# Performance work log

Hardware: AMD Instinct MI355X
Metric: run time of the kernel (lower is better)

Reference implementation:

```python
import jax, jax.numpy as jnp
import numpy as np

B, N, D, H, PSI = 8, 7225, 256, 8, 64
DH = D // H
DF = 4 * D
EPS = 1e-5


def _ln(x, g, b):
    m = jnp.mean(x, axis=-1, keepdims=True)
    v = jnp.mean((x - m) ** 2, axis=-1, keepdims=True)
    return (x - m) / jnp.sqrt(v + EPS) * g + b


def _gelu(x):
    return jax.nn.gelu(x, approximate=False)


def setup_inputs() -> dict:
    key = jax.random.key(0)
    ks = jax.random.split(key, 16)
    w = lambda k, s: (jax.random.normal(k, s, dtype=jnp.float32) * 0.02)
    inp = {
        'x': jax.random.normal(ks[0], (B, N, D), dtype=jnp.float32),
        'fx': jax.random.normal(ks[1], (B, N, D), dtype=jnp.float32),
        'ln1_g': jnp.ones((D,), jnp.float32), 'ln1_b': jnp.zeros((D,), jnp.float32),
        'Wq': w(ks[2], (D, D)), 'Wk': w(ks[3], (D, D)), 'Wv': w(ks[4], (D, D)),
        'Wo': w(ks[5], (D, D)), 'bo': jnp.zeros((D,), jnp.float32),
        'ln2_g': jnp.ones((D,), jnp.float32), 'ln2_b': jnp.zeros((D,), jnp.float32),
        'mlp_W1': w(ks[6], (D, DF)), 'mlp_b1': jnp.zeros((DF,), jnp.float32),
        'mlp_W2': w(ks[7], (DF, D)), 'mlp_b2': jnp.zeros((D,), jnp.float32),
        'proj_W1': w(ks[8], (D, D)), 'proj_b1': jnp.zeros((D,), jnp.float32),
        'proj_W2': w(ks[9], (D, PSI)), 'proj_b2': jnp.zeros((PSI,), jnp.float32),
        'mu': jnp.zeros((PSI,), jnp.float32),
        'ln3_g': jnp.ones((D,), jnp.float32), 'ln3_b': jnp.zeros((D,), jnp.float32),
        'mlp2_W1': w(ks[10], (D, DF)), 'mlp2_b1': jnp.zeros((DF,), jnp.float32),
        'mlp2_W2': w(ks[11], (DF, D)), 'mlp2_b2': jnp.zeros((D,), jnp.float32),
    }
    return inp


def _forward(x, fx, ln1_g, ln1_b, Wq, Wk, Wv, Wo, bo, ln2_g, ln2_b,
             mlp_W1, mlp_b1, mlp_W2, mlp_b2, proj_W1, proj_b1, proj_W2, proj_b2,
             mu, ln3_g, ln3_b, mlp2_W1, mlp2_b1, mlp2_W2, mlp2_b2):
    # --- linear (kernelized, non-causal) self-attention ---
    h = _ln(x, ln1_g, ln1_b)
    to_heads = lambda t: t.reshape(B, N, H, DH).transpose(0, 2, 1, 3)  # bhnd
    q = to_heads(h @ Wq)
    k = to_heads(h @ Wk)
    v = to_heads(h @ Wv)
    q = jax.nn.softmax(q, axis=-1) * (DH ** -0.5)   # feature-dim softmax
    k = jax.nn.softmax(k, axis=-2)                  # sequence-dim softmax
    ctx = jnp.einsum('bhnd,bhne->bhde', k, v)       # [B,H,DH,DH]
    attn = jnp.einsum('bhnd,bhde->bhne', q, ctx)    # [B,H,N,DH]
    attn = attn.transpose(0, 2, 1, 3).reshape(B, N, D) @ Wo + bo
    x = attn + x

    # --- MLP block (n_layers=0, no residual inside MLP) ---
    h = _ln(x, ln2_g, ln2_b)
    x = _gelu(h @ mlp_W1 + mlp_b1) @ mlp_W2 + mlp_b2 + x

    # --- low-rank projection + covariance whitening (orth=True, training path) ---
    x_ = _gelu(x @ proj_W1 + proj_b1) @ proj_W2 + proj_b2       # [B,N,PSI]
    cov = jnp.einsum('blc,bld->cd', x_, x_) / (B * N)           # [PSI,PSI]
    L = jnp.linalg.cholesky(cov)
    L_inv_T = jnp.linalg.inv(L).T
    x_ = x_ @ L_inv_T

    # --- softplus-scaled low-rank operator on fx ---
    ctx2 = jnp.einsum('blp,bld->bpd', x_, fx)                   # [B,PSI,D]
    fx = jnp.einsum('blp,bpd->bld', x_ * jax.nn.softplus(mu), ctx2)

    fx = _gelu(_ln(fx, ln3_g, ln3_b) @ mlp2_W1 + mlp2_b1) @ mlp2_W2 + mlp2_b2
    return x, fx


def reference(x, fx, ln1_g, ln1_b, Wq, Wk, Wv, Wo, bo, ln2_g, ln2_b,
              mlp_W1, mlp_b1, mlp_W2, mlp_b2, proj_W1, proj_b1, proj_W2, proj_b2,
              mu, ln3_g, ln3_b, mlp2_W1, mlp2_b1, mlp2_W2, mlp2_b2):
    return _forward(x, fx, ln1_g, ln1_b, Wq, Wk, Wv, Wo, bo, ln2_g, ln2_b,
                    mlp_W1, mlp_b1, mlp_W2, mlp_b2, proj_W1, proj_b1, proj_W2, proj_b2,
                    mu, ln3_g, ln3_b, mlp2_W1, mlp2_b1, mlp2_W2, mlp2_b2)
```

## Files before the change

kernel.cpp:

```cpp
#include <hip/hip_runtime.h>
#include <math.h>

typedef unsigned short u16;
typedef unsigned int u32;
typedef float f32x4 __attribute__((ext_vector_type(4)));
typedef __bf16 bf16x8 __attribute__((ext_vector_type(8)));

#define NTOK 57800
#define NSEQ 7225
#define NBATCH 8

static __device__ __forceinline__ float bf2f(u16 u){ u32 x=((u32)u)<<16; float f; __builtin_memcpy(&f,&x,4); return f; }
static __device__ __forceinline__ u16 f2bf(float f){ __bf16 h = (__bf16)f; u16 u; __builtin_memcpy(&u,&h,2); return u; }
static __device__ __forceinline__ float gelu_f(float v){
  float t = v * v;
  float w = fmaf(t, -0.07135481627f, -1.5957691216f);
  float e = __expf(w * v);
  return v * __builtin_amdgcn_rcpf(1.0f + e);
}

static __device__ __forceinline__ void gl16(const u16* g, u16* l){
  __builtin_amdgcn_global_load_lds((const __attribute__((address_space(1))) void*)g,
                                   (__attribute__((address_space(3))) void*)l, 16, 0, 0);
}

static __device__ __forceinline__ float rdlane(float v, int lane){
  int i; __builtin_memcpy(&i,&v,4);
  int r = __builtin_amdgcn_readlane(i, lane);
  float f; __builtin_memcpy(&f,&r,4);
  return f;
}

struct WJobs { const float* src[10]; u16* dst[10]; int K[10]; int N[10]; };
__global__ __launch_bounds__(256) void wtrans_all(WJobs j){
  int z = blockIdx.z;
  int K = j.K[z], N = j.N[z];
  int bk = blockIdx.x*32, bn = blockIdx.y*32;
  if (bk >= K || bn >= N) return;
  const float* src = j.src[z];
  u16* dst = j.dst[z];
  __shared__ float t[32][33];
  int tx = threadIdx.x&31, ty = threadIdx.x>>5;
  #pragma unroll
  for (int u=0;u<4;u++){
    int k = bk+ty+u*8, n = bn+tx;
    if (k<K && n<N) t[ty+u*8][tx] = src[(long)k*N+n];
  }
  __syncthreads();
  #pragma unroll
  for (int u=0;u<4;u++){
    int n = bn+ty+u*8, k = bk+tx;
    if (n<N && k<K) dst[(long)n*K+k] = f2bf(t[tx][ty+u*8]);
  }
}

__global__ __launch_bounds__(256) void ln_kernel(const float* __restrict__ in, const float* __restrict__ g,
                                                 const float* __restrict__ b, u16* __restrict__ out, int rows){
  int wid = threadIdx.x>>6, lane = threadIdx.x&63;
  int row = blockIdx.x*4 + wid;
  if (row >= rows) return;
  const float4 xv = *reinterpret_cast<const float4*>(in + (long)row*256 + lane*4);
  float s = xv.x+xv.y+xv.z+xv.w;
  float s2 = xv.x*xv.x+xv.y*xv.y+xv.z*xv.z+xv.w*xv.w;
  #pragma unroll
  for (int o=32;o;o>>=1){ s += __shfl_xor(s,o,64); s2 += __shfl_xor(s2,o,64); }
  float mean = s*(1.f/256.f);
  float var = fmaxf(s2*(1.f/256.f) - mean*mean, 0.f);
  float rstd = rsqrtf(var + 1e-5f);
  float4 gv = *reinterpret_cast<const float4*>(g + lane*4);
  float4 bv = *reinterpret_cast<const float4*>(b + lane*4);
  ushort4 o4;
  o4.x = f2bf((xv.x-mean)*rstd*gv.x + bv.x);
  o4.y = f2bf((xv.y-mean)*rstd*gv.y + bv.y);
  o4.z = f2bf((xv.z-mean)*rstd*gv.z + bv.z);
  o4.w = f2bf((xv.w-mean)*rstd*gv.w + bv.w);
  *reinterpret_cast<ushort4*>(out + (long)row*256 + lane*4) = o4;
}

template<bool BIASF, bool RESF, bool GELUF, bool OF32, bool OBF16>
__global__ __launch_bounds__(256) void gemm3(const u16* __restrict__ A, const u16* __restrict__ Bt,
    const float* __restrict__ bias, const float* __restrict__ resid,
    float* __restrict__ outF, u16* __restrict__ outB,
    int M, int N, int K, int gn, long aB, long bB, long cB)
{
  __shared__ __align__(16) u16 lds[2][8192];
  int nwg = gridDim.x, bid = blockIdx.x;
  int qx = nwg>>3, rx = nwg&7;
  int xcd = bid&7, lin = bid>>3;
  int swz = (xcd<rx)? (xcd*(qx+1)+lin) : (rx + xcd*qx + lin);
  int mi_ = swz/gn;
  int m0 = mi_*128, n0 = (swz - mi_*gn)*128;

  const u16* Ab  = A  + (long)blockIdx.z*aB;
  const u16* Btb = Bt + (long)blockIdx.z*bB;
  long coff = (long)blockIdx.z*cB;
  int tid = threadIdx.x, w = tid>>6, l = tid&63;
  int lr = l>>3;
  int csrc = (((l&7) ^ lr) << 3);
  int l15 = l&15, lq = l>>4;
  int wm = (w>>1)*64, wn = (w&1)*64;
  int sx = (l15&7)<<3;

  f32x4 acc[4][4];
  #pragma unroll
  for (int a=0;a<4;a++)
    #pragma unroll
    for (int b2=0;b2<4;b2++)
      #pragma unroll
      for (int r2=0;r2<4;r2++) acc[a][b2][r2]=0.f;

  int nt = K>>6;

  auto STAGE = [&](int k0){
    #pragma unroll
    for (int u=0;u<4;u++){
      int rr = w*32 + u*8;
      gl16(Ab  + (long)(m0+rr+lr)*K + k0 + csrc, &lds[0][0] + rr*64 + l*8);
      gl16(Btb + (long)(n0+rr+lr)*K + k0 + csrc, &lds[1][0] + rr*64 + l*8);
    }
  };

  STAGE(0);
  for (int t=0;;t++){
    __syncthreads();
    #pragma unroll
    for (int ks=0;ks<2;ks++){
      bf16x8 af[4], bfv[4];
      int ko = ks*32 + lq*8;
      #pragma unroll
      for (int mi=0;mi<4;mi++)
        af[mi]  = *reinterpret_cast<const bf16x8*>(&lds[0][0] + (wm+mi*16+l15)*64 + (ko ^ sx));
      #pragma unroll
      for (int ni=0;ni<4;ni++)
        bfv[ni] = *reinterpret_cast<const bf16x8*>(&lds[1][0] + (wn+ni*16+l15)*64 + (ko ^ sx));
      #pragma unroll
      for (int mi=0;mi<4;mi++)
        #pragma unroll
        for (int ni=0;ni<4;ni++)
          acc[mi][ni] = __builtin_amdgcn_mfma_f32_16x16x32_bf16(bfv[ni], af[mi], acc[mi][ni], 0,0,0);
    }
    if (t+1 == nt) break;
    __syncthreads();
    STAGE((t+1)<<6);
  }

  #pragma unroll
  for (int mi=0;mi<4;mi++){
    int row = m0 + wm + mi*16 + l15;
    if (row >= M) continue;
    #pragma unroll
    for (int ni=0;ni<4;ni++){
      int col0 = n0 + wn + ni*16 + lq*4;
      if (col0 >= N) continue;
      f32x4 v = acc[mi][ni];
      if (BIASF){
        const float4 bv = *reinterpret_cast<const float4*>(bias + col0);
        v[0]+=bv.x; v[1]+=bv.y; v[2]+=bv.z; v[3]+=bv.w;
      }
      long idx = (long)row*N + col0;
      if (RESF){
        const float4 rv = *reinterpret_cast<const float4*>(resid + coff + idx);
        v[0]+=rv.x; v[1]+=rv.y; v[2]+=rv.z; v[3]+=rv.w;
      }
      if (GELUF){
        #pragma unroll
        for (int r2=0;r2<4;r2++) v[r2] = gelu_f(v[r2]);
      }
      if (OF32){
        float4 o; o.x=v[0]; o.y=v[1]; o.z=v[2]; o.w=v[3];
        *reinterpret_cast<float4*>(outF + coff + idx) = o;
      }
      if (OBF16){
        ushort4 o; o.x=f2bf(v[0]); o.y=f2bf(v[1]); o.z=f2bf(v[2]); o.w=f2bf(v[3]);
        *reinterpret_cast<ushort4*>(outB + coff + idx) = o;
      }
    }
  }
}

template<bool RESF, bool OBF16>
__global__ __launch_bounds__(256) void mlp_fused(const u16* __restrict__ A,
    const u16* __restrict__ W1t, const float* __restrict__ b1,
    const u16* __restrict__ W2t, const float* __restrict__ b2,
    const float* __restrict__ resid, float* __restrict__ outF, u16* __restrict__ outB, int M)
{
  __shared__ __align__(16) u16 hA[4][4096];
  __shared__ __align__(16) u16 P[2][4096];
  int nwg = gridDim.x, bid = blockIdx.x;
  int qx = nwg>>3, rx = nwg&7;
  int xcd = bid&7, lin = bid>>3;
  int swz = (xcd<rx)? (xcd*(qx+1)+lin) : (rx + xcd*qx + lin);
  int m0 = swz*64;

  int tid = threadIdx.x, w = tid>>6, l = tid&63;
  int lr = l>>3;
  int csrc = (((l&7) ^ lr) << 3);
  int l15 = l&15, lq = l>>4;
  int sx = (l15&7)<<3;
  int jn1 = w*32;
  int nn2 = w*64;

  #pragma unroll
  for (int kc=0; kc<4; kc++){
    #pragma unroll
    for (int u=0; u<2; u++){
      int rr = w*16 + u*8;
      gl16(A + (long)(m0+rr+lr)*256 + kc*64 + csrc, &hA[kc][0] + rr*64 + l*8);
    }
  }

  f32x4 acc2[4][4];
  #pragma unroll
  for (int a=0;a<4;a++)
    #pragma unroll
    for (int b_=0;b_<4;b_++)
      #pragma unroll
      for (int r=0;r<4;r++) acc2[a][b_][r]=0.f;

  asm volatile("s_waitcnt vmcnt(0)" ::: "memory");
  __syncthreads();

  #pragma unroll 1
  for (int jb=0; jb<8; jb++){
    f32x4 acc1[4][2];
    #pragma unroll
    for (int a=0;a<4;a++)
      #pragma unroll
      for (int b_=0;b_<2;b_++)
        #pragma unroll
        for (int r=0;r<4;r++) acc1[a][b_][r]=0.f;
    __builtin_amdgcn_s_setprio(1);
    #pragma unroll
    for (int kc=0;kc<4;kc++){
      #pragma unroll
      for (int ks=0;ks<2;ks++){
        int ko = ks*32 + lq*8;
        bf16x8 af[4], bfv[2];
        #pragma unroll
        for (int ni=0;ni<2;ni++){
          int jrow = jb*128 + jn1 + ni*16 + l15;
          bfv[ni] = *reinterpret_cast<const bf16x8*>(W1t + (long)jrow*256 + kc*64 + ko);
        }
        #pragma unroll
        for (int mi=0;mi<4;mi++)
          af[mi] = *reinterpret_cast<const bf16x8*>(&hA[kc][0] + (mi*16+l15)*64 + (ko ^ sx));
        #pragma unroll
        for (int mi=0;mi<4;mi++)
          #pragma unroll
          for (int ni=0;ni<2;ni++)
            acc1[mi][ni] = __builtin_amdgcn_mfma_f32_16x16x32_bf16(bfv[ni], af[mi], acc1[mi][ni], 0,0,0);
      }
    }
    __builtin_amdgcn_s_setprio(0);
    #pragma unroll
    for (int mi=0;mi<4;mi++){
      int row = mi*16 + l15;
      #pragma unroll
      for (int ni=0;ni<2;ni++){
        int jj = jn1 + ni*16 + lq*4;
        const float4 bv = *reinterpret_cast<const float4*>(b1 + jb*128 + jj);
        f32x4 v = acc1[mi][ni];
        v[0] = gelu_f(v[0]+bv.x); v[1] = gelu_f(v[1]+bv.y);
        v[2] = gelu_f(v[2]+bv.z); v[3] = gelu_f(v[3]+bv.w);
        ushort4 o; o.x=f2bf(v[0]); o.y=f2bf(v[1]); o.z=f2bf(v[2]); o.w=f2bf(v[3]);
        int c = jj & 63, ch = jj >> 6;
        *reinterpret_cast<ushort4*>(&P[ch][0] + row*64 + (c ^ ((row&7)<<3))) = o;
      }
    }
    __syncthreads();
    __builtin_amdgcn_s_setprio(1);
    #pragma unroll
    for (int kk=0;kk<4;kk++){
      int ko = (kk&1)*32 + lq*8;
      int ch = kk>>1;
      bf16x8 af2[4], bf2v[4];
      #pragma unroll
      for (int ni=0;ni<4;ni++){
        int nrow = nn2 + ni*16 + l15;
        bf2v[ni] = *reinterpret_cast<const bf16x8*>(W2t + (long)nrow*1024 + jb*128 + kk*32 + lq*8);
      }
      #pragma unroll
      for (int mi=0;mi<4;mi++)
        af2[mi] = *reinterpret_cast<const bf16x8*>(&P[ch][0] + (mi*16+l15)*64 + (ko ^ sx));
      #pragma unroll
      for (int mi=0;mi<4;mi++)
        #pragma unroll
        for (int ni=0;ni<4;ni++)
          acc2[mi][ni] = __builtin_amdgcn_mfma_f32_16x16x32_bf16(bf2v[ni], af2[mi], acc2[mi][ni], 0,0,0);
    }
    __builtin_amdgcn_s_setprio(0);
    __syncthreads();
  }

  #pragma unroll
  for (int mi=0;mi<4;mi++){
    int row = m0 + mi*16 + l15;
    if (row >= M) continue;
    #pragma unroll
    for (int ni=0;ni<4;ni++){
      int col = nn2 + ni*16 + lq*4;
      f32x4 v = acc2[mi][ni];
      const float4 bv = *reinterpret_cast<const float4*>(b2 + col);
      v[0]+=bv.x; v[1]+=bv.y; v[2]+=bv.z; v[3]+=bv.w;
      long idx = (long)row*256 + col;
      if (RESF){
        const float4 rv = *reinterpret_cast<const float4*>(resid + idx);
        v[0]+=rv.x; v[1]+=rv.y; v[2]+=rv.z; v[3]+=rv.w;
      }
      float4 o; o.x=v[0]; o.y=v[1]; o.z=v[2]; o.w=v[3];
      *reinterpret_cast<float4*>(outF + idx) = o;
      if (OBF16){
        ushort4 ob; ob.x=f2bf(v[0]); ob.y=f2bf(v[1]); ob.z=f2bf(v[2]); ob.w=f2bf(v[3]);
        *reinterpret_cast<ushort4*>(outB + idx) = ob;
      }
    }
  }
}

__global__ __launch_bounds__(256) void ctx_part(const u16* __restrict__ qkvb, float* __restrict__ part,
                                                float* __restrict__ spart2){
  int ch = blockIdx.x, bh = blockIdx.y; int b = bh>>3, h = bh&7;
  __shared__ float ek[8][32], vl[8][32];
  int tid = threadIdx.x;
  int d = tid&31, eg = (tid>>5)*4;
  float acc[4] = {0.f,0.f,0.f,0.f};
  float ssum = 0.f;
  int n0 = ch*226; int n1 = n0+226; if (n1 > NSEQ) n1 = NSEQ;
  for (int nb=n0; nb<n1; nb+=8){
    #pragma unroll
    for (int u=0;u<2;u++){
      int idx = tid + u*256; int r = idx>>6, c = idx&63;
      int n = nb + r;
      if (c < 32) ek[r][c]    = (n<n1)? __expf(bf2f(qkvb[((long)(b*NSEQ+n))*768 + 256 + h*32 + c])) : 0.f;
      else        vl[r][c-32] = (n<n1)? bf2f(qkvb[((long)(b*NSEQ+n))*768 + 512 + h*32 + (c-32)]) : 0.f;
    }
    __syncthreads();
    #pragma unroll
    for (int r=0;r<8;r++){
      float kv = ek[r][d];
      ssum += kv;
      #pragma unroll
      for (int j=0;j<4;j++) acc[j] += kv * vl[r][eg+j];
    }
    __syncthreads();
  }
  #pragma unroll
  for (int j=0;j<4;j++) part[((long)(bh*32+ch))*1024 + d*32 + eg + j] = acc[j];
  if (tid < 32) spart2[(bh*32+ch)*32 + d] = ssum;
}
__global__ void ctx_red(const float* __restrict__ part, const float* __restrict__ spart2,
                        float* __restrict__ ctx){
  int bh = blockIdx.x;
  __shared__ float sinvl[32];
  int tid = threadIdx.x;
  if (tid < 32){
    float s=0.f;
    for (int ch=0;ch<32;ch++) s += spart2[(bh*32+ch)*32 + tid];
    sinvl[tid] = 1.0f/s;
  }
  __syncthreads();
  for (int idx=tid; idx<1024; idx+=256){
    float s=0.f;
    for (int ch=0;ch<32;ch++) s += part[((long)(bh*32+ch))*1024 + idx];
    ctx[(long)bh*1024 + idx] = s * sinvl[idx>>5];
  }
}

__global__ __launch_bounds__(256) void qsoftmax(const u16* __restrict__ qkvb, u16* __restrict__ qsb){
  int wid = threadIdx.x>>6, lane = threadIdx.x&63;
  int n = blockIdx.x*4 + wid;
  int b = blockIdx.y;
  if (n >= NSEQ) return;
  const ushort4 qv = *reinterpret_cast<const ushort4*>(qkvb + ((long)(b*NSEQ+n))*768 + lane*4);
  float e0 = __expf(bf2f(qv.x)), e1 = __expf(bf2f(qv.y)),
        e2 = __expf(bf2f(qv.z)), e3 = __expf(bf2f(qv.w));
  float s = e0+e1+e2+e3;
  s += __shfl_xor(s,1,64); s += __shfl_xor(s,2,64); s += __shfl_xor(s,4,64);
  float r = 0.17677669529663687f / s;
  ushort4 o; o.x=f2bf(e0*r); o.y=f2bf(e1*r); o.z=f2bf(e2*r); o.w=f2bf(e3*r);
  *reinterpret_cast<ushort4*>(qsb + ((long)(b*NSEQ+n))*256 + lane*4) = o;
}

__global__ __launch_bounds__(256) void ctx_wo(const float* __restrict__ ctx, const u16* __restrict__ wot,
                                              u16* __restrict__ w2bt){
  int jg = blockIdx.x, b = blockIdx.y;
  int j0 = jg*32;
  __shared__ u16 wol[32][256];
  int tid = threadIdx.x;
  {
    int r = tid>>3, c = (tid&7)*32;
    const uint4* src = reinterpret_cast<const uint4*>(wot + (j0+r)*256 + c);
    uint4* dst = reinterpret_cast<uint4*>(&wol[r][c]);
    dst[0]=src[0]; dst[1]=src[1]; dst[2]=src[2]; dst[3]=src[3];
  }
  int h = tid>>5, d = tid&31;
  float creg[32];
  {
    const float4* cp = reinterpret_cast<const float4*>(ctx + (long)(b*8+h)*1024 + d*32);
    #pragma unroll
    for (int u=0;u<8;u++){ float4 v = cp[u]; creg[u*4]=v.x; creg[u*4+1]=v.y; creg[u*4+2]=v.z; creg[u*4+3]=v.w; }
  }
  __syncthreads();
  for (int jj=0;jj<32;jj++){
    const uint4* wp = reinterpret_cast<const uint4*>(&wol[jj][h*32]);
    float acc = 0.f;
    #pragma unroll
    for (int u=0;u<4;u++){
      uint4 wv = wp[u];
      acc += bf2f((u16)(wv.x&0xffffu))*creg[u*8+0] + bf2f((u16)(wv.x>>16))*creg[u*8+1]
           + bf2f((u16)(wv.y&0xffffu))*creg[u*8+2] + bf2f((u16)(wv.y>>16))*creg[u*8+3]
           + bf2f((u16)(wv.z&0xffffu))*creg[u*8+4] + bf2f((u16)(wv.z>>16))*creg[u*8+5]
           + bf2f((u16)(wv.w&0xffffu))*creg[u*8+6] + bf2f((u16)(wv.w>>16))*creg[u*8+7];
    }
    w2bt[((long)b*256 + j0+jj)*256 + tid] = f2bf(acc);
  }
}

__global__ __launch_bounds__(256) void cov_part(const float* __restrict__ xu, float* __restrict__ part){
  int ch = blockIdx.x;
  __shared__ float xl[2][8][64];
  int tid = threadIdx.x;
  int i = tid&63, jg = (tid>>6)*16;
  int lrow = tid>>5, lcol = (tid&31)*2;
  float acc[16];
  #pragma unroll
  for (int j=0;j<16;j++) acc[j]=0.f;
  int n0 = ch*113;
  const int NT = 15;
  float2 xr2;
  auto LOAD = [&](int t){
    int n = n0 + t*8 + lrow;
    if (n < n0+113 && n < NTOK) xr2 = *reinterpret_cast<const float2*>(xu + (long)n*64 + lcol);
    else { xr2.x = 0.f; xr2.y = 0.f; }
  };
  LOAD(0);
  for (int t=0; t<NT; t++){
    int cur = t&1;
    xl[cur][lrow][lcol] = xr2.x; xl[cur][lrow][lcol+1] = xr2.y;
    __syncthreads();
    if (t+1 < NT) LOAD(t+1);
    #pragma unroll
    for (int r=0;r<8;r++){
      float xv = xl[cur][r][i];
      const float4* fb = reinterpret_cast<const float4*>(&xl[cur][r][jg]);
      float4 f0=fb[0], f1=fb[1], f2=fb[2], f3=fb[3];
      acc[0]+=xv*f0.x; acc[1]+=xv*f0.y; acc[2]+=xv*f0.z; acc[3]+=xv*f0.w;
      acc[4]+=xv*f1.x; acc[5]+=xv*f1.y; acc[6]+=xv*f1.z; acc[7]+=xv*f1.w;
      acc[8]+=xv*f2.x; acc[9]+=xv*f2.y; acc[10]+=xv*f2.z; acc[11]+=xv*f2.w;
      acc[12]+=xv*f3.x; acc[13]+=xv*f3.y; acc[14]+=xv*f3.z; acc[15]+=xv*f3.w;
    }
    __syncthreads();
  }
  #pragma unroll
  for (int j=0;j<16;j++) part[(long)ch*4096 + (jg+j)*64 + i] = acc[j];
}
__global__ void cov_red(const float* __restrict__ part, float* __restrict__ cov){
  __shared__ float red[4][64];
  int o = blockIdx.x*64 + (threadIdx.x&63);
  int sl = threadIdx.x>>6;
  float s=0.f;
  for (int ch=sl; ch<512; ch+=4) s += part[(long)ch*4096 + o];
  if (sl>0) red[sl][threadIdx.x&63] = s;
  __syncthreads();
  if (sl==0){
    s += red[1][threadIdx.x&63] + red[2][threadIdx.x&63] + red[3][threadIdx.x&63];
    cov[o] = s * (1.0f/57800.0f);
  }
}

__global__ __launch_bounds__(64) void chol_inv(const float* __restrict__ cov, float* __restrict__ Linv){
  int t = threadIdx.x;
  float r[64];
  #pragma unroll
  for (int k=0;k<16;k++){
    float4 v4 = *reinterpret_cast<const float4*>(cov + (long)t*64 + k*4);
    r[k*4]=v4.x; r[k*4+1]=v4.y; r[k*4+2]=v4.z; r[k*4+3]=v4.w;
  }
  float dinv[64];
  #pragma unroll
  for (int j=0;j<64;j++){
    float ajj = rdlane(r[j], j);
    float ljj = sqrtf(fmaxf(ajj, 1e-20f));
    float rinv = 1.0f / ljj;
    dinv[j] = rinv;
    float ltj = r[j] * rinv;
    r[j] = ltj;
    #pragma unroll
    for (int k=j+1;k<64;k++){
      float lkj = rdlane(ltj, k);
      r[k] -= ltj * lkj;
    }
  }
  float v[64];
  #pragma unroll
  for (int k=0;k<64;k++) v[k] = (k==t) ? 1.f : 0.f;
  #pragma unroll
  for (int i=0;i<64;i++){
    float xi = v[i] * dinv[i];
    Linv[i*64 + t] = xi;
    #pragma unroll
    for (int k=i+1;k<64;k++){
      v[k] -= rdlane(r[i], k) * xi;
    }
  }
}

__global__ __launch_bounds__(256) void whiten(const float* __restrict__ xu, const float* __restrict__ Linv,
                                              const float* __restrict__ mu, u16* __restrict__ xw, u16* __restrict__ xws){
  __shared__ float Ll[64][65];
  int tid = threadIdx.x;
  for (int u=0; u<16; u++){ int idx = u*256+tid; Ll[idx>>6][idx&63] = Linv[idx]; }
  __syncthreads();
  int wid = tid>>6, lane = tid&63;
  float m = mu[lane];
  float sp = (m > 20.f)? m : log1pf(expf(m));
  for (int rr=0; rr<4; rr++){
    int row = blockIdx.x*16 + wid*4 + rr;
    if (row >= NTOK) continue;
    float xj = xu[(long)row*64 + lane];
    float s = 0.f;
    #pragma unroll
    for (int j=0;j<64;j++) s += __shfl(xj, j, 64) * Ll[lane][j];
    xw[(long)row*64+lane]  = f2bf(s);
    xws[(long)row*64+lane] = f2bf(s * sp);
  }
}

__global__ __launch_bounds__(512) void ctx2_part(const u16* __restrict__ xw, const float* __restrict__ fx,
                                                 float* __restrict__ part){
  int ch = blockIdx.x, b = blockIdx.y;
  __shared__ float xwlf[2][16][64];
  __shared__ float fxl[2][16][256];
  int tid = threadIdx.x;
  int p = tid&63, jg = ((tid>>6)&7)*32;
  int lrow = tid>>5, lcol = (tid&31)*8, xcol = (tid&31)*2;
  float acc[32];
  #pragma unroll
  for (int j=0;j<32;j++) acc[j]=0.f;
  int n0 = ch*226;
  int n1 = n0+226; if (n1 > NSEQ) n1 = NSEQ;
  const int NT = 15;
  float4 fra, frb; u32 xr;
  auto LOAD = [&](int t){
    int n = n0 + t*16 + lrow;
    if (n < n1){
      const float4* fp = reinterpret_cast<const float4*>(fx + ((long)b*NSEQ+n)*256 + lcol);
      fra = fp[0]; frb = fp[1];
      xr = *reinterpret_cast<const u32*>(xw + ((long)b*NSEQ+n)*64 + xcol);
    } else {
      fra.x=0.f; fra.y=0.f; fra.z=0.f; fra.w=0.f;
      frb.x=0.f; frb.y=0.f; frb.z=0.f; frb.w=0.f;
      xr = 0;
    }
  };
  LOAD(0);
  for (int t=0; t<NT; t++){
    int cur = t&1;
    xwlf[cur][lrow][xcol]   = bf2f((u16)(xr&0xffffu));
    xwlf[cur][lrow][xcol+1] = bf2f((u16)(xr>>16));
    *reinterpret_cast<float4*>(&fxl[cur][lrow][lcol])   = fra;
    *reinterpret_cast<float4*>(&fxl[cur][lrow][lcol+4]) = frb;
    __syncthreads();
    if (t+1 < NT) LOAD(t+1);
    #pragma unroll
    for (int r=0;r<16;r++){
      float xv = xwlf[cur][r][p];
      const float4* fb = reinterpret_cast<const float4*>(&fxl[cur][r][jg]);
      #pragma unroll
      for (int c4=0;c4<8;c4++){
        float4 f = fb[c4];
        acc[c4*4+0]+=xv*f.x; acc[c4*4+1]+=xv*f.y; acc[c4*4+2]+=xv*f.z; acc[c4*4+3]+=xv*f.w;
      }
    }
    __syncthreads();
  }
  long base = ((long)(b*32+ch)*256 + jg)*64 + p;
  #pragma unroll
  for (int j=0;j<32;j++) part[base + (long)j*64] = acc[j];
}
__global__ void ctx2_red(const float* __restrict__ part, u16* __restrict__ c2t){
  int b = blockIdx.y;
  int idx0 = blockIdx.x*1024 + threadIdx.x;
  #pragma unroll
  for (int u=0;u<4;u++){
    int id = idx0 + u*256;
    float s=0.f;
    for (int ch=0;ch<32;ch++) s += part[(long)(b*32+ch)*16384 + id];
    c2t[(long)b*16384 + id] = f2bf(s);
  }
}

extern "C" void kernel_launch(void* const* d_in, const int* in_sizes, int n_in,
                              void* d_out, int out_size, void* d_ws, size_t ws_size,
                              hipStream_t stream)
{
  (void)in_sizes; (void)n_in; (void)out_size; (void)ws_size;
  const float* x     = (const float*)d_in[0];
  const float* fx    = (const float*)d_in[1];
  const float* ln1_g = (const float*)d_in[2];
  const float* ln1_b = (const float*)d_in[3];
  const float* Wq    = (const float*)d_in[4];
  const float* Wk    = (const float*)d_in[5];
  const float* Wv    = (const float*)d_in[6];
  const float* Wo    = (const float*)d_in[7];
  const float* bo    = (const float*)d_in[8];
  const float* ln2_g = (const float*)d_in[9];
  const float* ln2_b = (const float*)d_in[10];
  const float* mW1   = (const float*)d_in[11];
  const float* mb1   = (const float*)d_in[12];
  const float* mW2   = (const float*)d_in[13];
  const float* mb2   = (const float*)d_in[14];
  const float* pW1   = (const float*)d_in[15];
  const float* pb1   = (const float*)d_in[16];
  const float* pW2   = (const float*)d_in[17];
  const float* pb2   = (const float*)d_in[18];
  const float* mu    = (const float*)d_in[19];
  const float* ln3_g = (const float*)d_in[20];
  const float* ln3_b = (const float*)d_in[21];
  const float* m2W1  = (const float*)d_in[22];
  const float* m2b1  = (const float*)d_in[23];
  const float* m2W2  = (const float*)d_in[24];
  const float* m2b2  = (const float*)d_in[25];

  char* wsb = (char*)d_ws;
  u16* wt    = (u16*)wsb;
  u16* WQKVT = wt + 0;
  u16* WOT   = wt + 196608;
  u16* W1T   = wt + 262144;
  u16* W2T   = wt + 524288;
  u16* PW1T  = wt + 786432;
  u16* PW2T  = wt + 851968;
  u16* M2W1T = wt + 884736;
  u16* M2W2T = wt + 1146880;

  constexpr size_t OFF_H      = 2818048;
  constexpr size_t OFF_QKV    = 32440320;
  constexpr size_t OFF_ATT    = 150929408;
  constexpr size_t OFF_SPART2 = 180551680;
  constexpr size_t OFF_XU     = 180813824;
  constexpr size_t OFF_CTXP   = OFF_XU;
  constexpr size_t OFF_CTX    = OFF_XU + 8388608;
  constexpr size_t OFF_XW     = 195624960;
  constexpr size_t OFF_XWS    = 203023360;
  constexpr size_t OFF_W2BT   = 210430976;
  constexpr size_t OFF_COVP   = OFF_H;
  constexpr size_t OFF_COV    = OFF_H + 8388608;
  constexpr size_t OFF_LINV   = OFF_H + 8404992;
  constexpr size_t OFF_C2P    = OFF_QKV;
  constexpr size_t OFF_C2T    = OFF_QKV + 16777216;

  u16* h     = (u16*)(wsb + OFF_H);
  u16* qkvb  = (u16*)(wsb + OFF_QKV);
  u16* m1    = qkvb;
  u16* attb  = (u16*)(wsb + OFF_ATT);
  u16* qsb   = (u16*)(wsb + OFF_ATT);
  float* spart2= (float*)(wsb + OFF_SPART2);
  float* ctxp  = (float*)(wsb + OFF_CTXP);
  float* ctxb  = (float*)(wsb + OFF_CTX);
  float* xu    = (float*)(wsb + OFF_XU);
  u16*  xwb    = (u16*)(wsb + OFF_XW);
  u16*  xwsb   = (u16*)(wsb + OFF_XWS);
  float* covp  = (float*)(wsb + OFF_COVP);
  float* cov   = (float*)(wsb + OFF_COV);
  float* Linv  = (float*)(wsb + OFF_LINV);
  float* c2p   = (float*)(wsb + OFF_C2P);
  u16*  c2t    = (u16*)(wsb + OFF_C2T);
  u16*  w2bt   = (u16*)(wsb + OFF_W2BT);

  float* outx  = (float*)d_out;
  float* outfx = outx + 14796800;

  WJobs wj;
  wj.src[0]=Wq;   wj.dst[0]=WQKVT;          wj.K[0]=256;  wj.N[0]=256;
  wj.src[1]=Wk;   wj.dst[1]=WQKVT+65536;    wj.K[1]=256;  wj.N[1]=256;
  wj.src[2]=Wv;   wj.dst[2]=WQKVT+131072;   wj.K[2]=256;  wj.N[2]=256;
  wj.src[3]=Wo;   wj.dst[3]=WOT;            wj.K[3]=256;  wj.N[3]=256;
  wj.src[4]=mW1;  wj.dst[4]=W1T;            wj.K[4]=256;  wj.N[4]=1024;
  wj.src[5]=mW2;  wj.dst[5]=W2T;            wj.K[5]=1024; wj.N[5]=256;
  wj.src[6]=pW1;  wj.dst[6]=PW1T;           wj.K[6]=256;  wj.N[6]=256;
  wj.src[7]=pW2;  wj.dst[7]=PW2T;           wj.K[7]=256;  wj.N[7]=64;
  wj.src[8]=m2W1; wj.dst[8]=M2W1T;          wj.K[8]=256;  wj.N[8]=1024;
  wj.src[9]=m2W2; wj.dst[9]=M2W2T;          wj.K[9]=1024; wj.N[9]=256;
  wtrans_all<<<dim3(32,32,10),256,0,stream>>>(wj);

  ln_kernel<<<14450,256,0,stream>>>(x, ln1_g, ln1_b, h, NTOK);
  gemm3<false,false,false,false,true><<<dim3(452*6,1,1),256,0,stream>>>(
      h, WQKVT, nullptr, nullptr, nullptr, qkvb, NTOK, 768, 256, 6, 0,0,0);
  qsoftmax<<<dim3(1807,8),256,0,stream>>>(qkvb, qsb);
  ctx_part<<<dim3(32,64),256,0,stream>>>(qkvb, ctxp, spart2);
  ctx_red<<<64,256,0,stream>>>(ctxp, spart2, ctxb);
  ctx_wo<<<dim3(8,8),256,0,stream>>>(ctxb, WOT, w2bt);
  gemm3<true,true,false,true,false><<<dim3(57*2,1,8),256,0,stream>>>(
      qsb, w2bt, bo, x, outx, nullptr, NSEQ, 256, 256, 2,
      (long)NSEQ*256, 256*256, (long)NSEQ*256);

  ln_kernel<<<14450,256,0,stream>>>(outx, ln2_g, ln2_b, h, NTOK);
  gemm3<true,false,true,false,true><<<dim3(452*8,1,1),256,0,stream>>>(
      h, W1T, mb1, nullptr, nullptr, m1, NTOK, 1024, 256, 8, 0,0,0);
  gemm3<true,true,false,true,true><<<dim3(452*2,1,1),256,0,stream>>>(
      m1, W2T, mb2, outx, outx, attb, NTOK, 256, 1024, 2, 0,0,0);

  gemm3<true,false,true,false,true><<<dim3(452*2,1,1),256,0,stream>>>(
      attb, PW1T, pb1, nullptr, nullptr, h, NTOK, 256, 256, 2, 0,0,0);
  gemm3<true,false,false,true,false><<<dim3(452,1,1),256,0,stream>>>(
      h, PW2T, pb2, nullptr, xu, nullptr, NTOK, 64, 256, 1, 0,0,0);

  cov_part<<<512,256,0,stream>>>(xu, covp);
  cov_red<<<64,256,0,stream>>>(covp, cov);
  chol_inv<<<1,64,0,stream>>>(cov, Linv);
  whiten<<<3613,256,0,stream>>>(xu, Linv, mu, xwb, xwsb);

  ctx2_part<<<dim3(32,8),512,0,stream>>>(xwb, fx, c2p);
  ctx2_red<<<dim3(16,8),256,0,stream>>>(c2p, c2t);
  gemm3<false,false,false,true,false><<<dim3(57*2,1,8),256,0,stream>>>(
      xwsb, c2t, nullptr, nullptr, outfx, nullptr, NSEQ, 256, 64, 2,
      (long)NSEQ*64, 256*64, (long)NSEQ*256);

  ln_kernel<<<14450,256,0,stream>>>(outfx, ln3_g, ln3_b, h, NTOK);
  mlp_fused<false,false><<<904,256,0,stream>>>(h, M2W1T, m2b1, M2W2T, m2b2, nullptr, outfx, nullptr, NTOK);
}
```

Before: 840.0 us.

## Add K=256 specialized GEMM and unfuse second MLP into two GEMMs

Replaces the fused MLP kernel with a new gemmK256 kernel that preloads the full 128x256 A tile into LDS and reads B directly from global memory. The new kernel is used for all K=256 GEMMs in place of the generic gemm3. The second MLP now runs as two GEMMs through the m1 intermediate buffer. The aim is fewer K-loop syncs and better MMA throughput, at the cost of an extra round trip of the 1024-wide hidden activation through memory.

```diff
diff --git a/kernel.cpp b/kernel.cpp
--- a/kernel.cpp
+++ b/kernel.cpp
@@ -178,140 +178,97 @@
   }
 }
 
-template<bool RESF, bool OBF16>
-__global__ __launch_bounds__(256) void mlp_fused(const u16* __restrict__ A,
-    const u16* __restrict__ W1t, const float* __restrict__ b1,
-    const u16* __restrict__ W2t, const float* __restrict__ b2,
-    const float* __restrict__ resid, float* __restrict__ outF, u16* __restrict__ outB, int M)
+template<bool BIASF, bool RESF, bool GELUF, bool OF32, bool OBF16>
+__global__ __launch_bounds__(256) void gemmK256(const u16* __restrict__ A, const u16* __restrict__ Bt,
+    const float* __restrict__ bias, const float* __restrict__ resid,
+    float* __restrict__ outF, u16* __restrict__ outB,
+    int M, int N, int gn, long aB, long bB, long cB)
 {
-  __shared__ __align__(16) u16 hA[4][4096];
-  __shared__ __align__(16) u16 P[2][4096];
+  __shared__ __align__(16) u16 hA[4][8192];
   int nwg = gridDim.x, bid = blockIdx.x;
   int qx = nwg>>3, rx = nwg&7;
   int xcd = bid&7, lin = bid>>3;
   int swz = (xcd<rx)? (xcd*(qx+1)+lin) : (rx + xcd*qx + lin);
-  int m0 = swz*64;
-
+  int mi_ = swz/gn;
+  int m0 = mi_*128, n0 = (swz - mi_*gn)*128;
+
+  const u16* Ab  = A  + (long)blockIdx.z*aB;
+  const u16* Btb = Bt + (long)blockIdx.z*bB;
+  long coff = (long)blockIdx.z*cB;
   int tid = threadIdx.x, w = tid>>6, l = tid&63;
   int lr = l>>3;
   int csrc = (((l&7) ^ lr) << 3);
   int l15 = l&15, lq = l>>4;
+  int wm = (w>>1)*64, wn = (w&1)*64;
   int sx = (l15&7)<<3;
-  int jn1 = w*32;
-  int nn2 = w*64;
 
   #pragma unroll
   for (int kc=0; kc<4; kc++){
     #pragma unroll
-    for (int u=0; u<2; u++){
-      int rr = w*16 + u*8;
-      gl16(A + (long)(m0+rr+lr)*256 + kc*64 + csrc, &hA[kc][0] + rr*64 + l*8);
-    }
-  }
-
-  f32x4 acc2[4][4];
+    for (int u=0; u<4; u++){
+      int rr = w*32 + u*8;
+      gl16(Ab + (long)(m0+rr+lr)*256 + kc*64 + csrc, &hA[kc][0] + rr*64 + l*8);
+    }
+  }
+
+  f32x4 acc[4][4];
   #pragma unroll
   for (int a=0;a<4;a++)
     #pragma unroll
-    for (int b_=0;b_<4;b_++)
-      #pragma unroll
-      for (int r=0;r<4;r++) acc2[a][b_][r]=0.f;
+    for (int b2=0;b2<4;b2++)
+      #pragma unroll
+      for (int r2=0;r2<4;r2++) acc[a][b2][r2]=0.f;
 
   asm volatile("s_waitcnt vmcnt(0)" ::: "memory");
   __syncthreads();
 
-  #pragma unroll 1
-  for (int jb=0; jb<8; jb++){
-    f32x4 acc1[4][2];
-    #pragma unroll
-    for (int a=0;a<4;a++)
-      #pragma unroll
-      for (int b_=0;b_<2;b_++)
+  #pragma unroll
+  for (int ks=0; ks<8; ks++){
+    int kc = ks>>1;
+    int ko = (ks&1)*32 + lq*8;
+    bf16x8 af[4], bfv[4];
+    #pragma unroll
+    for (int ni=0;ni<4;ni++)
+      bfv[ni] = *reinterpret_cast<const bf16x8*>(Btb + (long)(n0+wn+ni*16+l15)*256 + ks*32 + lq*8);
+    #pragma unroll
+    for (int mi=0;mi<4;mi++)
+      af[mi] = *reinterpret_cast<const bf16x8*>(&hA[kc][0] + (wm+mi*16+l15)*64 + (ko ^ sx));
+    #pragma unroll
+    for (int mi=0;mi<4;mi++)
+      #pragma unroll
+      for (int ni=0;ni<4;ni++)
+        acc[mi][ni] = __builtin_amdgcn_mfma_f32_16x16x32_bf16(bfv[ni], af[mi], acc[mi][ni], 0,0,0);
+  }
+
+  #pragma unroll
+  for (int mi=0;mi<4;mi++){
+    int row = m0 + wm + mi*16 + l15;
+    if (row >= M) continue;
+    #pragma unroll
+    for (int ni=0;ni<4;ni++){
+      int col0 = n0 + wn + ni*16 + lq*4;
+      if (col0 >= N) continue;
+      f32x4 v = acc[mi][ni];
+      if (BIASF){
+        const float4 bv = *reinterpret_cast<const float4*>(bias + col0);
+        v[0]+=bv.x; v[1]+=bv.y; v[2]+=bv.z; v[3]+=bv.w;
+      }
+      long idx = (long)row*N + col0;
+      if (RESF){
+        const float4 rv = *reinterpret_cast<const float4*>(resid + coff + idx);
+        v[0]+=rv.x; v[1]+=rv.y; v[2]+=rv.z; v[3]+=rv.w;
+      }
+      if (GELUF){
         #pragma unroll
-        for (int r=0;r<4;r++) acc1[a][b_][r]=0.f;
-    __builtin_amdgcn_s_setprio(1);
-    #pragma unroll
-    for (int kc=0;kc<4;kc++){
-      #pragma unroll
-      for (int ks=0;ks<2;ks++){
-        int ko = ks*32 + lq*8;
-        bf16x8 af[4], bfv[2];
-        #pragma unroll
-        for (int ni=0;ni<2;ni++){
-          int jrow = jb*128 + jn1 + ni*16 + l15;
-          bfv[ni] = *reinterpret_cast<const bf16x8*>(W1t + (long)jrow*256 + kc*64 + ko);
-        }
-        #pragma unroll
-        for (int mi=0;mi<4;mi++)
-          af[mi] = *reinterpret_cast<const bf16x8*>(&hA[kc][0] + (mi*16+l15)*64 + (ko ^ sx));
-        #pragma unroll
-        for (int mi=0;mi<4;mi++)
-          #pragma unroll
-          for (int ni=0;ni<2;ni++)
-            acc1[mi][ni] = __builtin_amdgcn_mfma_f32_16x16x32_bf16(bfv[ni], af[mi], acc1[mi][ni], 0,0,0);
-      }
-    }
-    __builtin_amdgcn_s_setprio(0);
-    #pragma unroll
-    for (int mi=0;mi<4;mi++){
-      int row = mi*16 + l15;
-      #pragma unroll
-      for (int ni=0;ni<2;ni++){
-        int jj = jn1 + ni*16 + lq*4;
-        const float4 bv = *reinterpret_cast<const float4*>(b1 + jb*128 + jj);
-        f32x4 v = acc1[mi][ni];
-        v[0] = gelu_f(v[0]+bv.x); v[1] = gelu_f(v[1]+bv.y);
-        v[2] = gelu_f(v[2]+bv.z); v[3] = gelu_f(v[3]+bv.w);
+        for (int r2=0;r2<4;r2++) v[r2] = gelu_f(v[r2]);
+      }
+      if (OF32){
+        float4 o; o.x=v[0]; o.y=v[1]; o.z=v[2]; o.w=v[3];
+        *reinterpret_cast<float4*>(outF + coff + idx) = o;
+      }
+      if (OBF16){
         ushort4 o; o.x=f2bf(v[0]); o.y=f2bf(v[1]); o.z=f2bf(v[2]); o.w=f2bf(v[3]);
-        int c = jj & 63, ch = jj >> 6;
-        *reinterpret_cast<ushort4*>(&P[ch][0] + row*64 + (c ^ ((row&7)<<3))) = o;
-      }
-    }
-    __syncthreads();
-    __builtin_amdgcn_s_setprio(1);
-    #pragma unroll
-    for (int kk=0;kk<4;kk++){
-      int ko = (kk&1)*32 + lq*8;
-      int ch = kk>>1;
-      bf16x8 af2[4], bf2v[4];
-      #pragma unroll
-      for (int ni=0;ni<4;ni++){
-        int nrow = nn2 + ni*16 + l15;
-        bf2v[ni] = *reinterpret_cast<const bf16x8*>(W2t + (long)nrow*1024 + jb*128 + kk*32 + lq*8);
-      }
-      #pragma unroll
-      for (int mi=0;mi<4;mi++)
-        af2[mi] = *reinterpret_cast<const bf16x8*>(&P[ch][0] + (mi*16+l15)*64 + (ko ^ sx));
-      #pragma unroll
-      for (int mi=0;mi<4;mi++)
-        #pragma unroll
-        for (int ni=0;ni<4;ni++)
-          acc2[mi][ni] = __builtin_amdgcn_mfma_f32_16x16x32_bf16(bf2v[ni], af2[mi], acc2[mi][ni], 0,0,0);
-    }
-    __builtin_amdgcn_s_setprio(0);
-    __syncthreads();
-  }
-
-  #pragma unroll
-  for (int mi=0;mi<4;mi++){
-    int row = m0 + mi*16 + l15;
-    if (row >= M) continue;
-    #pragma unroll
-    for (int ni=0;ni<4;ni++){
-      int col = nn2 + ni*16 + lq*4;
-      f32x4 v = acc2[mi][ni];
-      const float4 bv = *reinterpret_cast<const float4*>(b2 + col);
-      v[0]+=bv.x; v[1]+=bv.y; v[2]+=bv.z; v[3]+=bv.w;
-      long idx = (long)row*256 + col;
-      if (RESF){
-        const float4 rv = *reinterpret_cast<const float4*>(resid + idx);
-        v[0]+=rv.x; v[1]+=rv.y; v[2]+=rv.z; v[3]+=rv.w;
-      }
-      float4 o; o.x=v[0]; o.y=v[1]; o.z=v[2]; o.w=v[3];
-      *reinterpret_cast<float4*>(outF + idx) = o;
-      if (OBF16){
-        ushort4 ob; ob.x=f2bf(v[0]); ob.y=f2bf(v[1]); ob.z=f2bf(v[2]); ob.w=f2bf(v[3]);
-        *reinterpret_cast<ushort4*>(outB + idx) = ob;
+        *reinterpret_cast<ushort4*>(outB + coff + idx) = o;
       }
     }
   }
@@ -684,26 +641,26 @@
   wtrans_all<<<dim3(32,32,10),256,0,stream>>>(wj);
 
   ln_kernel<<<14450,256,0,stream>>>(x, ln1_g, ln1_b, h, NTOK);
-  gemm3<false,false,false,false,true><<<dim3(452*6,1,1),256,0,stream>>>(
-      h, WQKVT, nullptr, nullptr, nullptr, qkvb, NTOK, 768, 256, 6, 0,0,0);
+  gemmK256<false,false,false,false,true><<<dim3(452*6,1,1),256,0,stream>>>(
+      h, WQKVT, nullptr, nullptr, nullptr, qkvb, NTOK, 768, 6, 0,0,0);
   qsoftmax<<<dim3(1807,8),256,0,stream>>>(qkvb, qsb);
   ctx_part<<<dim3(32,64),256,0,stream>>>(qkvb, ctxp, spart2);
   ctx_red<<<64,256,0,stream>>>(ctxp, spart2, ctxb);
   ctx_wo<<<dim3(8,8),256,0,stream>>>(ctxb, WOT, w2bt);
-  gemm3<true,true,false,true,false><<<dim3(57*2,1,8),256,0,stream>>>(
-      qsb, w2bt, bo, x, outx, nullptr, NSEQ, 256, 256, 2,
+  gemmK256<true,true,false,true,false><<<dim3(57*2,1,8),256,0,stream>>>(
+      qsb, w2bt, bo, x, outx, nullptr, NSEQ, 256, 2,
       (long)NSEQ*256, 256*256, (long)NSEQ*256);
 
   ln_kernel<<<14450,256,0,stream>>>(outx, ln2_g, ln2_b, h, NTOK);
-  gemm3<true,false,true,false,true><<<dim3(452*8,1,1),256,0,stream>>>(
-      h, W1T, mb1, nullptr, nullptr, m1, NTOK, 1024, 256, 8, 0,0,0);
+  gemmK256<true,false,true,false,true><<<dim3(452*8,1,1),256,0,stream>>>(
+      h, W1T, mb1, nullptr, nullptr, m1, NTOK, 1024, 8, 0,0,0);
   gemm3<true,true,false,true,true><<<dim3(452*2,1,1),256,0,stream>>>(
       m1, W2T, mb2, outx, outx, attb, NTOK, 256, 1024, 2, 0,0,0);
 
-  gemm3<true,false,true,false,true><<<dim3(452*2,1,1),256,0,stream>>>(
-      attb, PW1T, pb1, nullptr, nullptr, h, NTOK, 256, 256, 2, 0,0,0);
-  gemm3<true,false,false,true,false><<<dim3(452,1,1),256,0,stream>>>(
-      h, PW2T, pb2, nullptr, xu, nullptr, NTOK, 64, 256, 1, 0,0,0);
+  gemmK256<true,false,true,false,true><<<dim3(452*2,1,1),256,0,stream>>>(
+      attb, PW1T, pb1, nullptr, nullptr, h, NTOK, 256, 2, 0,0,0);
+  gemmK256<true,false,false,true,false><<<dim3(452,1,1),256,0,stream>>>(
+      h, PW2T, pb2, nullptr, xu, nullptr, NTOK, 64, 1, 0,0,0);
 
   cov_part<<<512,256,0,stream>>>(xu, covp);
   cov_red<<<64,256,0,stream>>>(covp, cov);
@@ -717,5 +674,8 @@
       (long)NSEQ*64, 256*64, (long)NSEQ*256);
 
   ln_kernel<<<14450,256,0,stream>>>(outfx, ln3_g, ln3_b, h, NTOK);
-  mlp_fused<false,false><<<904,256,0,stream>>>(h, M2W1T, m2b1, M2W2T, m2b2, nullptr, outfx, nullptr, NTOK);
-}
+  gemmK256<true,false,true,false,true><<<dim3(452*8,1,1),256,0,stream>>>(
+      h, M2W1T, m2b1, nullptr, nullptr, m1, NTOK, 1024, 8, 0,0,0);
+  gemm3<true,false,false,true,false><<<dim3(452*2,1,1),256,0,stream>>>(
+      m1, M2W2T, m2b2, nullptr, outfx, nullptr, NTOK, 256, 1024, 2, 0,0,0);
+}
```

After: 893.8 us. +6.4%, slower.
